# Optimization experiments

Measured on AMD Instinct MI355X. Metric: run time of the kernel, lower is better.

Reference implementation:

```python
import jax, jax.numpy as jnp
import numpy as np

N = 100000
E = 1600000
G = 64  # number of graphs
H = 128
BN_EPS = 1e-5


def setup_inputs() -> dict:
    key = jax.random.key(0)
    ks = jax.random.split(key, 12)
    x = jax.random.normal(ks[0], (N, 3), dtype=jnp.float32)
    edge_index = jax.random.randint(ks[1], (2, E), 0, N, dtype=jnp.int64)
    batch = jnp.sort(jax.random.randint(ks[2], (N,), 0, G, dtype=jnp.int64))
    W1 = jax.random.normal(ks[3], (3, H), dtype=jnp.float32) * 0.3
    W2 = jax.random.normal(ks[4], (H, H), dtype=jnp.float32) * 0.05
    W3 = jax.random.normal(ks[5], (H, H), dtype=jnp.float32) * 0.05
    lin_W = jax.random.normal(ks[6], (H, 2), dtype=jnp.float32) * 0.05
    d = {
        'x': x, 'edge_index': edge_index, 'batch': batch,
        'W1': W1, 'b1': jnp.zeros((H,), jnp.float32),
        'W2': W2, 'b2': jnp.zeros((H,), jnp.float32),
        'W3': W3, 'b3': jnp.zeros((H,), jnp.float32),
        'lin_W': lin_W, 'lin_b': jnp.zeros((2,), jnp.float32),
    }
    for i, kk in zip((1, 2, 3), ks[7:10]):
        d[f'bn{i}_g'] = jnp.ones((H,), jnp.float32)
        d[f'bn{i}_b'] = jnp.zeros((H,), jnp.float32)
        d[f'bn{i}_m'] = jnp.zeros((H,), jnp.float32)
        d[f'bn{i}_v'] = jax.random.uniform(kk, (H,), dtype=jnp.float32, minval=0.5, maxval=1.5)
    return d


def _gcn(x, src, dst, norm, W, b):
    # GCNConv: out = scatter_add(norm * (xW)[src], dst) + b
    h = x @ W
    msg = h[src] * norm[:, None]
    agg = jax.ops.segment_sum(msg, dst, num_segments=N)
    return agg + b


def _bn_eval(x, g, b, m, v):
    return (x - m) * jax.lax.rsqrt(v + BN_EPS) * g + b


def reference(x, edge_index, batch, W1, b1, W2, b2, W3, b3,
              bn1_g, bn1_b, bn1_m, bn1_v,
              bn2_g, bn2_b, bn2_m, bn2_v,
              bn3_g, bn3_b, bn3_m, bn3_v,
              lin_W, lin_b):
    loop = jnp.arange(N, dtype=edge_index.dtype)
    src = jnp.concatenate([edge_index[0], loop])
    dst = jnp.concatenate([edge_index[1], loop])
    # symmetric normalization with self-loops: deg from destination nodes
    deg = jax.ops.segment_sum(jnp.ones_like(dst, dtype=x.dtype), dst, num_segments=N)
    dinv = jnp.where(deg > 0, jax.lax.rsqrt(deg), 0.0)
    norm = dinv[src] * dinv[dst]

    h = jax.nn.relu(_bn_eval(_gcn(x, src, dst, norm, W1, b1), bn1_g, bn1_b, bn1_m, bn1_v))
    h = jax.nn.relu(_bn_eval(_gcn(h, src, dst, norm, W2, b2), bn2_g, bn2_b, bn2_m, bn2_v))
    h = jax.nn.relu(_bn_eval(_gcn(h, src, dst, norm, W3, b3), bn3_g, bn3_b, bn3_m, bn3_v))
    # dropout is identity in eval mode
    sums = jax.ops.segment_sum(h, batch, num_segments=G)
    cnts = jax.ops.segment_sum(jnp.ones((N,), h.dtype), batch, num_segments=G)
    pooled = sums / jnp.maximum(cnts, 1.0)[:, None]
    return pooled @ lin_W + lin_b
```

## Files before the change

### kernel.cpp

```cpp
#include <hip/hip_runtime.h>

#define NN 100000
#define EE 1600000
#define GG 64
#define HH 128
#define BN_EPS 1e-5f

#define CB 782
#define NB 256
#define TILE 6250

typedef unsigned short ushort_t;
typedef __attribute__((ext_vector_type(8))) short bf16x8;
typedef __attribute__((ext_vector_type(4))) float f32x4;

#define MFMA16 __builtin_amdgcn_mfma_f32_16x16x32_bf16

#define WFRAG_LO 16384

static __device__ inline ushort_t f2bf(float f) {
    unsigned u = __float_as_uint(f);
    unsigned r = (u + 0x7FFF + ((u >> 16) & 1)) >> 16;
    return (ushort_t)r;
}
static __device__ inline float bf2f(ushort_t b) {
    return __uint_as_float(((unsigned)b) << 16);
}


__global__ __launch_bounds__(256) void k_hist(const int* __restrict__ ei,
                                              int* __restrict__ histG) {
    __shared__ int h[CB];
    int t = threadIdx.x;
    for (int i = t; i < CB; i += 256) h[i] = 0;
    __syncthreads();
    int e0 = blockIdx.x * TILE;
    for (int i = t; i < TILE; i += 256) {
        int d = ei[EE + e0 + i];
        atomicAdd(&h[d >> 7], 1);
    }
    __syncthreads();
    for (int i = t; i < CB; i += 256) histG[blockIdx.x * CB + i] = h[i];
}

__global__ __launch_bounds__(NB) void k_bscan(int* __restrict__ histG,
                                              int* __restrict__ total) {
    __shared__ int sh[NB];
    int t = threadIdx.x;
    int c = blockIdx.x;
    sh[t] = histG[t * CB + c];
    __syncthreads();
    for (int d = 1; d < NB; d <<= 1) {
        int x = (t >= d) ? sh[t - d] : 0;
        __syncthreads();
        sh[t] += x;
        __syncthreads();
    }
    histG[t * CB + c] = (t > 0) ? sh[t - 1] : 0;
    if (t == NB - 1) total[c] = sh[NB - 1];
}

__global__ __launch_bounds__(1024) void k_cbase(const int* __restrict__ total,
                                                int* __restrict__ cbase) {
    __shared__ int sh[1024];
    int t = threadIdx.x;
    sh[t] = (t < CB) ? total[t] : 0;
    __syncthreads();
    for (int d = 1; d < 1024; d <<= 1) {
        int x = (t >= d) ? sh[t - d] : 0;
        __syncthreads();
        sh[t] += x;
        __syncthreads();
    }
    if (t < CB) cbase[t] = (t > 0) ? sh[t - 1] : 0;
    if (t == CB - 1) cbase[CB] = sh[t];
}

__global__ __launch_bounds__(256) void k_cscatter(const int* __restrict__ ei,
                                                  const int* __restrict__ histG,
                                                  const int* __restrict__ cbase,
                                                  int* __restrict__ metaS) {
    __shared__ int base_l[CB];
    __shared__ int cur_l[CB];
    int t = threadIdx.x;
    int b = blockIdx.x;
    for (int i = t; i < CB; i += 256) {
        base_l[i] = cbase[i] + histG[b * CB + i];
        cur_l[i] = 0;
    }
    __syncthreads();
    int e0 = b * TILE;
    for (int i = t; i < TILE; i += 256) {
        int s = ei[e0 + i];
        int d = ei[EE + e0 + i];
        int c = d >> 7;
        int p = base_l[c] + atomicAdd(&cur_l[c], 1);
        metaS[p] = s | ((d & 127) << 17);
    }
}

__global__ __launch_bounds__(256) void k_fine(const int* __restrict__ metaS,
                                              const int* __restrict__ cbase,
                                              int* __restrict__ cnt,
                                              int* __restrict__ offs,
                                              int* __restrict__ col,
                                              float* __restrict__ dinv) {
    __shared__ int hist[128];
    __shared__ int scn[128];
    __shared__ int cur[128];
    int t = threadIdx.x;
    int c = blockIdx.x;
    int lo = cbase[c], hi = cbase[c + 1];
    if (t < 128) hist[t] = 0;
    __syncthreads();
    for (int r = lo + t; r < hi; r += 256) atomicAdd(&hist[metaS[r] >> 17], 1);
    __syncthreads();
    if (t < 128) scn[t] = hist[t];
    __syncthreads();
    for (int d = 1; d < 128; d <<= 1) {
        int x = (t >= d && t < 128) ? scn[t - d] : 0;
        __syncthreads();
        if (t < 128) scn[t] += x;
        __syncthreads();
    }
    if (t < 128) {
        int excl = (t > 0) ? scn[t - 1] : 0;
        cur[t] = excl;
        int node = c * 128 + t;
        if (node < NN) {
            cnt[node] = hist[t];
            offs[node] = lo + excl;
            dinv[node] = rsqrtf((float)(hist[t] + 1));
        }
    }
    __syncthreads();
    for (int r = lo + t; r < hi; r += 256) {
        int pk = metaS[r];
        int s = pk & 0x1FFFF;
        int idx = atomicAdd(&cur[pk >> 17], 1);
        col[lo + idx] = s;
    }
}


__global__ __launch_bounds__(256) void k_wprep(const float* __restrict__ W2,
                                               const float* __restrict__ W3,
                                               ushort_t* __restrict__ w2f,
                                               ushort_t* __restrict__ w3f,
                                               const int* __restrict__ batch,
                                               int* __restrict__ gcnt) {
    if (blockIdx.x == 16) {
        int g = threadIdx.x;
        if (g < 64) {
            int lo = 0, hi = NN;
            while (lo < hi) { int mid = (lo + hi) >> 1; if (batch[mid] < g) lo = mid + 1; else hi = mid; }
            int a = lo;
            lo = 0; hi = NN;
            int g1 = g + 1;
            while (lo < hi) { int mid = (lo + hi) >> 1; if (batch[mid] < g1) lo = mid + 1; else hi = mid; }
            gcnt[g] = lo - a;
        }
        return;
    }
    const float* W = (blockIdx.x & 8) ? W3 : W2;
    ushort_t* o = (blockIdx.x & 8) ? w3f : w2f;
    int tid = ((int)blockIdx.x & 7) * 256 + threadIdx.x;
    int l = tid & 63;
    int kb = ((tid >> 6) & 3) * 32 + (l >> 4) * 8;
    int n = (tid >> 8) * 16 + (l & 15);
    unsigned hp[4], lp[4];
#pragma unroll
    for (int p = 0; p < 4; p++) {
        float v0 = W[(size_t)(kb + 2 * p) * HH + n];
        float v1 = W[(size_t)(kb + 2 * p + 1) * HH + n];
        ushort_t h0 = f2bf(v0), h1 = f2bf(v1);
        ushort_t l0 = f2bf(v0 - bf2f(h0)), l1 = f2bf(v1 - bf2f(h1));
        hp[p] = (unsigned)h0 | ((unsigned)h1 << 16);
        lp[p] = (unsigned)l0 | ((unsigned)l1 << 16);
    }
    *(uint4*)&o[(size_t)tid * 8] = make_uint4(hp[0], hp[1], hp[2], hp[3]);
    *(uint4*)&o[WFRAG_LO + (size_t)tid * 8] = make_uint4(lp[0], lp[1], lp[2], lp[3]);
}


__global__ __launch_bounds__(256) void k_aggx(const float* __restrict__ x,
                                              const int* __restrict__ offs,
                                              const int* __restrict__ cnt,
                                              const int* __restrict__ col,
                                              const float* __restrict__ dinv,
                                              float* __restrict__ wgt,
                                              float4* __restrict__ agg) {
    int tid = threadIdx.x;
    int wave = tid >> 6;
    int lane = tid & 63;
    int grp = lane >> 4;
    int l = lane & 15;
    int n = blockIdx.x * 16 + wave * 4 + grp;
    float dv = dinv[n];
    int base = offs[n], cn = cnt[n];
    float a0 = 0.f, a1 = 0.f, a2 = 0.f;
    for (int i = l; i < cn; i += 16) {
        int s = col[base + i];
        float w = dinv[s] * dv;
        wgt[base + i] = w;
        a0 += w * x[s * 3 + 0];
        a1 += w * x[s * 3 + 1];
        a2 += w * x[s * 3 + 2];
    }
#pragma unroll
    for (int off = 8; off >= 1; off >>= 1) {
        a0 += __shfl_xor(a0, off, 16);
        a1 += __shfl_xor(a1, off, 16);
        a2 += __shfl_xor(a2, off, 16);
    }
    if (l == 0) {
        float w0 = dv * dv;
        a0 += w0 * x[n * 3 + 0];
        a1 += w0 * x[n * 3 + 1];
        a2 += w0 * x[n * 3 + 2];
        agg[n] = make_float4(a0, a1, a2, 0.f);
    }
}


__global__ __launch_bounds__(256) void k_mml1(const float4* __restrict__ agg,
                                              const float* __restrict__ W1,
                                              const float* __restrict__ b1,
                                              const float* __restrict__ g1,
                                              const float* __restrict__ bb1,
                                              const float* __restrict__ m1,
                                              const float* __restrict__ v1,
                                              const ushort_t* __restrict__ Wf,
                                              ushort_t* __restrict__ outB) {
    __shared__ float4 ag[64];
    __shared__ __align__(16) ushort_t xh[2][64 * HH];
    int tid = threadIdx.x;
    int row0 = blockIdx.x * 64;
    if (tid < 64) {
        int gr = row0 + tid;
        ag[tid] = (gr < NN) ? agg[gr] : make_float4(0.f, 0.f, 0.f, 0.f);
    }
    __syncthreads();
    {
        int c = tid & 127;
        int rh = tid >> 7;
        float w0 = W1[c], w1 = W1[128 + c], w2 = W1[256 + c];
        float sc = g1[c] * rsqrtf(v1[c] + BN_EPS);
        float sh = (b1[c] - m1[c]) * sc + bb1[c];
#pragma unroll
        for (int i = 0; i < 32; i++) {
            int r = 2 * i + rh;
            float4 a = ag[r];
            float t = fmaxf((a.x * w0 + a.y * w1 + a.z * w2) * sc + sh, 0.f);
            ushort_t hi = f2bf(t);
            ushort_t lo = f2bf(t - bf2f(hi));
            int idx = r * HH + (c ^ ((r & 7) << 3));
            xh[0][idx] = hi;
            xh[1][idx] = lo;
        }
    }
    __syncthreads();

    int w = tid >> 6, l = tid & 63;
    int r_lo = l & 15, kgrp = l >> 4;
    int row_l = w * 16 + r_lo;
    f32x4 acc[8];
#pragma unroll
    for (int nt = 0; nt < 8; nt++) acc[nt] = (f32x4){0.f, 0.f, 0.f, 0.f};

#pragma unroll
    for (int kk = 0; kk < 4; kk++) {
        int ke = kk * 32 + kgrp * 8;
        int idx = row_l * HH + (ke ^ ((row_l & 7) << 3));
        bf16x8 ahf = *(const bf16x8*)&xh[0][idx];
        bf16x8 alf = *(const bf16x8*)&xh[1][idx];
#pragma unroll
        for (int nt = 0; nt < 8; nt++) {
            int fo = ((((nt << 2) | kk) << 6) + l) * 8;
            bf16x8 bh = *(const bf16x8*)&Wf[fo];
            bf16x8 bl = *(const bf16x8*)&Wf[WFRAG_LO + fo];
            acc[nt] = MFMA16(ahf, bh, acc[nt], 0, 0, 0);
            acc[nt] = MFMA16(ahf, bl, acc[nt], 0, 0, 0);
            acc[nt] = MFMA16(alf, bh, acc[nt], 0, 0, 0);
        }
    }
#pragma unroll
    for (int q = 0; q < 4; q++) {
        int gr = row0 + w * 16 + kgrp * 4 + q;
        if (gr < NN) {
            size_t rb = (size_t)gr * HH + r_lo;
#pragma unroll
            for (int nt = 0; nt < 8; nt++)
                outB[rb + nt * 16] = f2bf(acc[nt][q]);
        }
    }
}


__global__ __launch_bounds__(256) void k_mm(const ushort_t* __restrict__ xin,
                                            const ushort_t* __restrict__ Wf,
                                            ushort_t* __restrict__ outB) {
    int tid = threadIdx.x;
    int w = tid >> 6, l = tid & 63;
    int row0 = blockIdx.x * 128 + w * 32;
    int r_lo = l & 15, kgrp = l >> 4;
    f32x4 acc[2][8];
#pragma unroll
    for (int rt = 0; rt < 2; rt++)
#pragma unroll
        for (int nt = 0; nt < 8; nt++) acc[rt][nt] = (f32x4){0.f, 0.f, 0.f, 0.f};

    bf16x8 za = {0, 0, 0, 0, 0, 0, 0, 0};
#pragma unroll
    for (int kk = 0; kk < 4; kk++) {
        int ke = kk * 32 + kgrp * 8;
        int ra0 = row0 + r_lo;
        int ra1 = row0 + 16 + r_lo;
        bf16x8 a0 = (ra0 < NN) ? *(const bf16x8*)&xin[(size_t)ra0 * HH + ke] : za;
        bf16x8 a1 = (ra1 < NN) ? *(const bf16x8*)&xin[(size_t)ra1 * HH + ke] : za;
#pragma unroll
        for (int nt = 0; nt < 8; nt++) {
            int fo = ((((nt << 2) | kk) << 6) + l) * 8;
            bf16x8 bh = *(const bf16x8*)&Wf[fo];
            bf16x8 bl = *(const bf16x8*)&Wf[WFRAG_LO + fo];
            acc[0][nt] = MFMA16(a0, bh, acc[0][nt], 0, 0, 0);
            acc[0][nt] = MFMA16(a0, bl, acc[0][nt], 0, 0, 0);
            acc[1][nt] = MFMA16(a1, bh, acc[1][nt], 0, 0, 0);
            acc[1][nt] = MFMA16(a1, bl, acc[1][nt], 0, 0, 0);
        }
    }
#pragma unroll
    for (int rt = 0; rt < 2; rt++)
#pragma unroll
        for (int q = 0; q < 4; q++) {
            int gr = row0 + rt * 16 + kgrp * 4 + q;
            if (gr < NN) {
                size_t rb = (size_t)gr * HH + r_lo;
#pragma unroll
                for (int nt = 0; nt < 8; nt++)
                    outB[rb + nt * 16] = f2bf(acc[rt][nt][q]);
            }
        }
}


__global__ __launch_bounds__(256) void k_agg(const ushort_t* __restrict__ t,
                                             const int* __restrict__ offs,
                                             const int* __restrict__ cnt,
                                             const int* __restrict__ col,
                                             const float* __restrict__ wgt,
                                             const float* __restrict__ dinv,
                                             const float* __restrict__ bias,
                                             const float* __restrict__ g,
                                             const float* __restrict__ bb,
                                             const float* __restrict__ m,
                                             const float* __restrict__ v,
                                             ushort_t* __restrict__ out) {
    int wave = threadIdx.x >> 6;
    int lane = threadIdx.x & 63;
    int half = lane >> 5;
    int l = lane & 31;
    int d = blockIdx.x * 8 + wave * 2 + half;
    int c0 = l * 4;
    float dv = dinv[d];
    float w0 = dv * dv;
    ushort4 selfR = *(const ushort4*)&t[(size_t)d * HH + c0];
    float4 acc;
    acc.x = bf2f(selfR.x) * w0; acc.y = bf2f(selfR.y) * w0;
    acc.z = bf2f(selfR.z) * w0; acc.w = bf2f(selfR.w) * w0;
    int base = offs[d], cn = cnt[d];
    for (int ib = 0; ib < cn; ib += 32) {
        int i = ib + l;
        int s = 0;
        float w = 0.f;
        if (i < cn) {
            s = col[base + i];
            w = wgt[base + i];
        }
        int lim = min(32, cn - ib);
#pragma unroll 8
        for (int j = 0; j < lim; j++) {
            int ss = __shfl(s, j, 32);
            float ww = __shfl(w, j, 32);
            ushort4 tv = *(const ushort4*)&t[(size_t)ss * HH + c0];
            acc.x += ww * bf2f(tv.x);
            acc.y += ww * bf2f(tv.y);
            acc.z += ww * bf2f(tv.z);
            acc.w += ww * bf2f(tv.w);
        }
    }
    float4 gg = *(const float4*)&g[c0];
    float4 vv = *(const float4*)&v[c0];
    float4 mm = *(const float4*)&m[c0];
    float4 bv = *(const float4*)&bb[c0];
    float4 bi = *(const float4*)&bias[c0];
    float sc0 = gg.x * rsqrtf(vv.x + BN_EPS);
    float sc1 = gg.y * rsqrtf(vv.y + BN_EPS);
    float sc2 = gg.z * rsqrtf(vv.z + BN_EPS);
    float sc3 = gg.w * rsqrtf(vv.w + BN_EPS);
    ushort4 o;
    o.x = f2bf(fmaxf(acc.x * sc0 + (bi.x - mm.x) * sc0 + bv.x, 0.f));
    o.y = f2bf(fmaxf(acc.y * sc1 + (bi.y - mm.y) * sc1 + bv.y, 0.f));
    o.z = f2bf(fmaxf(acc.z * sc2 + (bi.z - mm.z) * sc2 + bv.z, 0.f));
    o.w = f2bf(fmaxf(acc.w * sc3 + (bi.w - mm.w) * sc3 + bv.w, 0.f));
    *(ushort4*)&out[(size_t)d * HH + c0] = o;
}


#define PBLK 3125
__global__ void k_pool(const ushort_t* __restrict__ h, const int* __restrict__ batch,
                       float* __restrict__ gsum) {
    int c = threadIdx.x;
    int n0 = blockIdx.x * 32;
    int n1 = n0 + 32;
    float acc = 0.f;
    int cur = batch[n0];
    for (int n = n0; n < n1; n++) {
        int gr = batch[n];
        if (gr != cur) {
            atomicAdd(&gsum[cur * HH + c], acc);
            acc = 0.f; cur = gr;
        }
        acc += bf2f(h[(size_t)n * HH + c]);
    }
    atomicAdd(&gsum[cur * HH + c], acc);
}


__global__ void k_head(const float* __restrict__ gsum, const int* __restrict__ gcnt,
                       const float* __restrict__ linW, const float* __restrict__ linb,
                       float* __restrict__ out) {
    int t = threadIdx.x;
    int gr = t >> 1, j = t & 1;
    float inv = 1.0f / fmaxf((float)gcnt[gr], 1.0f);
    float acc = 0.f;
    for (int c = 0; c < HH; c++) acc += gsum[gr * HH + c] * linW[c * 2 + j];
    out[t] = acc * inv + linb[j];
}


static inline size_t al256(size_t x) { return (x + 255) & ~(size_t)255; }

extern "C" void kernel_launch(void* const* d_in, const int* in_sizes, int n_in,
                              void* d_out, int out_size, void* d_ws, size_t ws_size,
                              hipStream_t stream) {
    const float* x    = (const float*)d_in[0];
    const int*   ei   = (const int*)d_in[1];
    const int*   batch= (const int*)d_in[2];
    const float* W1   = (const float*)d_in[3];
    const float* b1   = (const float*)d_in[4];
    const float* W2   = (const float*)d_in[5];
    const float* b2   = (const float*)d_in[6];
    const float* W3   = (const float*)d_in[7];
    const float* b3   = (const float*)d_in[8];
    const float* linW = (const float*)d_in[9];
    const float* linb = (const float*)d_in[10];
    const float* bn1g = (const float*)d_in[11];
    const float* bn1b = (const float*)d_in[12];
    const float* bn1m = (const float*)d_in[13];
    const float* bn1v = (const float*)d_in[14];
    const float* bn2g = (const float*)d_in[15];
    const float* bn2b = (const float*)d_in[16];
    const float* bn2m = (const float*)d_in[17];
    const float* bn2v = (const float*)d_in[18];
    const float* bn3g = (const float*)d_in[19];
    const float* bn3b = (const float*)d_in[20];
    const float* bn3m = (const float*)d_in[21];
    const float* bn3v = (const float*)d_in[22];
    float* out = (float*)d_out;

    char* ws = (char*)d_ws;
    size_t off = 0;
    int*    histG  = (int*)(ws + off);    off += al256((size_t)NB * CB * 4);
    int*    total  = (int*)(ws + off);    off += al256((size_t)CB * 4);
    int*    cbase  = (int*)(ws + off);    off += al256((size_t)(CB + 1) * 4);
    int*    cnt    = (int*)(ws + off);    off += al256((size_t)NN * 4);
    int*    offs   = (int*)(ws + off);    off += al256((size_t)NN * 4);
    float*  dinv   = (float*)(ws + off);  off += al256((size_t)NN * 4);
    int*    col    = (int*)(ws + off);    off += al256((size_t)EE * 4);
    float*  wgt    = (float*)(ws + off);  off += al256((size_t)EE * 4);
    ushort_t* w2f  = (ushort_t*)(ws + off); off += al256((size_t)2 * WFRAG_LO * 2);
    ushort_t* w3f  = (ushort_t*)(ws + off); off += al256((size_t)2 * WFRAG_LO * 2);
    float4* agg    = (float4*)(ws + off); off += al256((size_t)NN * 16);
    char*   bufA   = (char*)(ws + off);   off += al256((size_t)NN * HH * 2);
    char*   bufB   = (char*)(ws + off);   off += al256((size_t)NN * HH * 4);
    float*  gsum   = (float*)(ws + off);  off += (size_t)GG * HH * 4;
    int*    gcnt   = (int*)(ws + off);    off += al256((size_t)GG * 4);

    int* metaS = (int*)bufB;
    ushort_t* tB = (ushort_t*)bufB;
    ushort_t* hB = (ushort_t*)bufA;

    hipMemsetAsync(gsum, 0, (size_t)GG * HH * 4, stream);

    k_wprep<<<17, 256, 0, stream>>>(W2, W3, w2f, w3f, batch, gcnt);

    k_hist<<<NB, 256, 0, stream>>>(ei, histG);
    k_bscan<<<CB, NB, 0, stream>>>(histG, total);
    k_cbase<<<1, 1024, 0, stream>>>(total, cbase);
    k_cscatter<<<NB, 256, 0, stream>>>(ei, histG, cbase, metaS);
    k_fine<<<CB, 256, 0, stream>>>(metaS, cbase, cnt, offs, col, dinv);

    k_aggx<<<NN / 16, 256, 0, stream>>>(x, offs, cnt, col, dinv, wgt, agg);

    k_mml1<<<(NN + 63) / 64, 256, 0, stream>>>(agg, W1, b1, bn1g, bn1b, bn1m, bn1v,
                                               w2f, tB);
    k_agg<<<NN / 8, 256, 0, stream>>>(tB, offs, cnt, col, wgt, dinv,
                                      b2, bn2g, bn2b, bn2m, bn2v, hB);

    k_mm<<<(NN + 127) / 128, 256, 0, stream>>>(hB, w3f, tB);
    k_agg<<<NN / 8, 256, 0, stream>>>(tB, offs, cnt, col, wgt, dinv,
                                      b3, bn3g, bn3b, bn3m, bn3v, hB);

    k_pool<<<PBLK, 128, 0, stream>>>(hB, batch, gsum);
    k_head<<<1, 128, 0, stream>>>(gsum, gcnt, linW, linb, out);
}
```

Baseline: 402.3 us.

## Locally sort edges by coarse bucket in LDS before scattering to global

The coarse-bucket scatter now first counts per-bucket ranks in shared memory, runs a block-wide prefix scan, and places each tile's packed edges in bucket order in LDS. It then writes to global with consecutive threads hitting mostly consecutive addresses, replacing the random scattered stores. The tile size changes to 6400 edges over 250 blocks, so each thread holds exactly 25 edges in registers, and the block scan is padded to 256 threads. The cost is extra LDS (about 55KB per block), more registers, and additional barriers.

Result: faster. 393.6 us (-2.2%).

```diff
diff --git a/kernel.cpp b/kernel.cpp
--- a/kernel.cpp
+++ b/kernel.cpp
@@ -7,8 +7,9 @@
 #define BN_EPS 1e-5f
 
 #define CB 782
-#define NB 256
-#define TILE 6250
+#define NB 250
+#define TILE 6400
+#define EPT 25
 
 typedef unsigned short ushort_t;
 typedef __attribute__((ext_vector_type(8))) short bf16x8;
@@ -43,21 +44,21 @@
     for (int i = t; i < CB; i += 256) histG[blockIdx.x * CB + i] = h[i];
 }
 
-__global__ __launch_bounds__(NB) void k_bscan(int* __restrict__ histG,
-                                              int* __restrict__ total) {
-    __shared__ int sh[NB];
+__global__ __launch_bounds__(256) void k_bscan(int* __restrict__ histG,
+                                               int* __restrict__ total) {
+    __shared__ int sh[256];
     int t = threadIdx.x;
     int c = blockIdx.x;
-    sh[t] = histG[t * CB + c];
-    __syncthreads();
-    for (int d = 1; d < NB; d <<= 1) {
+    sh[t] = (t < NB) ? histG[t * CB + c] : 0;
+    __syncthreads();
+    for (int d = 1; d < 256; d <<= 1) {
         int x = (t >= d) ? sh[t - d] : 0;
         __syncthreads();
         sh[t] += x;
         __syncthreads();
     }
-    histG[t * CB + c] = (t > 0) ? sh[t - 1] : 0;
-    if (t == NB - 1) total[c] = sh[NB - 1];
+    if (t < NB) histG[t * CB + c] = (t > 0) ? sh[t - 1] : 0;
+    if (t == 255) total[c] = sh[255];
 }
 
 __global__ __launch_bounds__(1024) void k_cbase(const int* __restrict__ total,
@@ -81,21 +82,57 @@
                                                   const int* __restrict__ cbase,
                                                   int* __restrict__ metaS) {
     __shared__ int base_l[CB];
-    __shared__ int cur_l[CB];
+    __shared__ int cnt_l[1024];
+    __shared__ int part[256];
+    __shared__ int srt[TILE];
+    __shared__ int ga[TILE];
     int t = threadIdx.x;
     int b = blockIdx.x;
-    for (int i = t; i < CB; i += 256) {
+    for (int i = t; i < CB; i += 256)
         base_l[i] = cbase[i] + histG[b * CB + i];
-        cur_l[i] = 0;
-    }
+    for (int i = t; i < 1024; i += 256) cnt_l[i] = 0;
     __syncthreads();
     int e0 = b * TILE;
-    for (int i = t; i < TILE; i += 256) {
+    int cs[EPT], rs[EPT], ps[EPT];
+#pragma unroll
+    for (int k = 0; k < EPT; k++) {
+        int i = t + k * 256;
         int s = ei[e0 + i];
         int d = ei[EE + e0 + i];
         int c = d >> 7;
-        int p = base_l[c] + atomicAdd(&cur_l[c], 1);
-        metaS[p] = s | ((d & 127) << 17);
+        cs[k] = c;
+        rs[k] = atomicAdd(&cnt_l[c], 1);
+        ps[k] = s | ((d & 127) << 17);
+    }
+    __syncthreads();
+    int v0 = cnt_l[t * 4], v1 = cnt_l[t * 4 + 1];
+    int v2 = cnt_l[t * 4 + 2], v3 = cnt_l[t * 4 + 3];
+    part[t] = v0 + v1 + v2 + v3;
+    __syncthreads();
+    for (int d = 1; d < 256; d <<= 1) {
+        int x = (t >= d) ? part[t - d] : 0;
+        __syncthreads();
+        part[t] += x;
+        __syncthreads();
+    }
+    int excl = (t > 0) ? part[t - 1] : 0;
+    cnt_l[t * 4]     = excl;
+    cnt_l[t * 4 + 1] = excl + v0;
+    cnt_l[t * 4 + 2] = excl + v0 + v1;
+    cnt_l[t * 4 + 3] = excl + v0 + v1 + v2;
+    __syncthreads();
+#pragma unroll
+    for (int k = 0; k < EPT; k++) {
+        int c = cs[k];
+        int slot = cnt_l[c] + rs[k];
+        srt[slot] = ps[k];
+        ga[slot] = base_l[c] + rs[k];
+    }
+    __syncthreads();
+#pragma unroll
+    for (int k = 0; k < EPT; k++) {
+        int i = t + k * 256;
+        metaS[ga[i]] = srt[i];
     }
 }
 
@@ -496,7 +533,7 @@
     k_wprep<<<17, 256, 0, stream>>>(W2, W3, w2f, w3f, batch, gcnt);
 
     k_hist<<<NB, 256, 0, stream>>>(ei, histG);
-    k_bscan<<<CB, NB, 0, stream>>>(histG, total);
+    k_bscan<<<CB, 256, 0, stream>>>(histG, total);
     k_cbase<<<1, 1024, 0, stream>>>(total, cbase);
     k_cscatter<<<NB, 256, 0, stream>>>(ei, histG, cbase, metaS);
     k_fine<<<CB, 256, 0, stream>>>(metaS, cbase, cnt, offs, col, dinv);
```
